# Optimization experiments

Hardware: AMD Instinct MI355X
Metric: run time of the kernel (lower is better)

## Reference

```python
import jax, jax.numpy as jnp
import numpy as np

B, T, E, H = 4, 1024, 1024, 16
D = E // H  # head_dim = 64


def setup_inputs() -> dict:
    key = jax.random.key(0)
    ks = jax.random.split(key, 6)
    s = 0.02  # realistic init scale for stable softmax
    return {
        "hidden_states": jax.random.normal(ks[0], (B, T, E), jnp.float32),
        "attention_mask": jnp.zeros((B, 1, T, T), jnp.float32),
        "Wq": jax.random.normal(ks[1], (E, E), jnp.float32) * s,
        "bq": jnp.zeros((E,), jnp.float32),
        "Wk": jax.random.normal(ks[2], (E, E), jnp.float32) * s,
        "bk": jnp.zeros((E,), jnp.float32),
        "Wv": jax.random.normal(ks[3], (E, E), jnp.float32) * s,
        "bv": jnp.zeros((E,), jnp.float32),
        "Wo": jax.random.normal(ks[4], (E, E), jnp.float32) * s,
        "bo": jnp.zeros((E,), jnp.float32),
    }


def reference(hidden_states, attention_mask, Wq, bq, Wk, bk, Wv, bv, Wo, bo):
    b, t, e = hidden_states.shape
    scaling = jnp.asarray(D, hidden_states.dtype) ** -0.5
    # q_proj weights/bias are pre-scaled in the module; equivalent to scaling q output
    q = (hidden_states @ Wq.T + bq) * scaling      # [B,T,E]
    k = hidden_states @ Wk.T + bk                   # self-attention path (no cache)
    v = hidden_states @ Wv.T + bv
    q = q.reshape(b, t, H, D)
    k = k.reshape(b, t, H, D)
    v = v.reshape(b, t, H, D)
    # bmm(q, k^T): [B,H,T,S] score matrix (materialized, as in the original)
    scores = jnp.einsum("bthd,bshd->bhts", q, k) + attention_mask
    probs = jax.nn.softmax(scores, axis=-1)
    ctx = jnp.einsum("bhts,bshd->bthd", probs, v).reshape(b, t, e)
    return ctx @ Wo.T + bo
```

## Files before the change

kernel.cpp:

```cpp
#include <hip/hip_runtime.h>
#include <math.h>

#define BB 4
#define TT 1024
#define EE 1024
#define HH 16
#define DD 64
#define KDIM 1024
#define N_HS (4096 * 1024)
#define N_W  (1024 * 1024)
#define NQKV (BB * HH * TT * DD)
#define LOG2E 1.44269504088896340736f

typedef _Float16 f16x8 __attribute__((ext_vector_type(8)));
typedef _Float16 f16x4 __attribute__((ext_vector_type(4)));
typedef _Float16 f16x2 __attribute__((ext_vector_type(2)));
typedef float    f32x4 __attribute__((ext_vector_type(4)));

__device__ __forceinline__ unsigned short f2h(float x) {
    _Float16 h = (_Float16)x;
    return __builtin_bit_cast(unsigned short, h);
}
__device__ __forceinline__ void split_h(float x, unsigned short& hi, unsigned short& lo) {
    _Float16 h = (_Float16)x;
    hi = __builtin_bit_cast(unsigned short, h);
    lo = f2h(x - (float)h);
}

__device__ __forceinline__ f16x2 cvt_pk(float a, float b) {
    return __builtin_bit_cast(f16x2, __builtin_amdgcn_cvt_pkrtz(a, b));
}

__device__ __forceinline__ void gload16(const void* g, void* l) {
    __builtin_amdgcn_global_load_lds(
        (const __attribute__((address_space(1))) void*)g,
        (__attribute__((address_space(3))) void*)l, 16, 0, 0);
}

__device__ __forceinline__ float mx3(float a, float b, float c) {
    return fmaxf(fmaxf(a, b), c);
}

__global__ __launch_bounds__(256)
void split_kernel(const float* __restrict__ hs,
                  const float* __restrict__ Wq, const float* __restrict__ Wk,
                  const float* __restrict__ Wv, const float* __restrict__ Wo,
                  const float* __restrict__ mask, int* __restrict__ mflag,
                  unsigned short* __restrict__ ws)
{
    const int u = blockIdx.x * 256 + threadIdx.x;
    if (u < (N_HS / 4) + N_W) {
        const float* src;
        unsigned short* dst;
        if (u < (N_HS / 4)) {
            src = hs + (size_t)u * 4;
            dst = ws + (size_t)u * 4;
        } else {
            int v = u - N_HS / 4;
            int wsel = v >> 18;
            int wo   = v & 0x3FFFF;
            const float* Wsrc = (wsel == 0) ? Wq : (wsel == 1) ? Wk : (wsel == 2) ? Wv : Wo;
            src = Wsrc + (size_t)wo * 4;
            dst = ws + (size_t)N_HS + (size_t)wsel * N_W + (size_t)wo * 4;
        }
        float4 x = *(const float4*)src;
        ushort4 h4;
        h4.x = f2h(x.x); h4.y = f2h(x.y); h4.z = f2h(x.z); h4.w = f2h(x.w);
        *(ushort4*)dst = h4;
    } else {
        int v = u - ((N_HS / 4) + N_W);
        float4 x = *(const float4*)(mask + (size_t)v * 4);
        bool nz = (x.x != 0.f) || (x.y != 0.f) || (x.z != 0.f) || (x.w != 0.f);
        if (__any(nz) && (threadIdx.x & 63) == 0)
            atomicOr(mflag, 1);
    }
}

__global__ __launch_bounds__(256)
void qkv_kernel(const unsigned short* __restrict__ hsp,
                const unsigned short* __restrict__ wqp,
                const float* __restrict__ bq, const float* __restrict__ bk,
                const float* __restrict__ bv,
                unsigned short* __restrict__ qkvb)
{
    __shared__ unsigned short Ah[128 * 32], Bh[128 * 32];

    const int widx  = blockIdx.x >> 3;
    const int nbase = (blockIdx.x & 7) * 128;
    const int mbase = blockIdx.y * 128;
    const unsigned short* Wp = wqp + (size_t)widx * N_W;
    const float* bias = (widx == 0) ? bq : (widx == 1) ? bk : bv;
    unsigned short* dst = qkvb + (size_t)widx * NQKV;
    const float scale = (widx == 0) ? 0.125f * LOG2E : 1.0f;

    const int tid  = threadIdx.x;
    const int w    = tid >> 6;
    const int lane = tid & 63;
    const int quad = lane >> 4;
    const int l16  = lane & 15;
    const int wm   = (w >> 1) * 64;
    const int wn   = (w & 1) * 64;

    f32x4 acc[4][4];
#pragma unroll
    for (int i = 0; i < 4; i++)
#pragma unroll
        for (int j = 0; j < 4; j++) acc[i][j] = (f32x4)0.f;

#pragma unroll 1
    for (int kt = 0; kt < KDIM; kt += 32) {
        __syncthreads();
#pragma unroll
        for (int i = 0; i < 2; i++) {
            int u = tid + i * 256;
            int r = u >> 2, c = u & 3;
            int q = c ^ ((r >> 1) & 3);
            gload16(hsp + (size_t)(mbase + r) * KDIM + kt + q * 8, &Ah[u * 8]);
            gload16(Wp  + (size_t)(nbase + r) * KDIM + kt + q * 8, &Bh[u * 8]);
        }
        __syncthreads();

        f16x8 af[4], bfr[4];
#pragma unroll
        for (int i = 0; i < 4; i++) {
            int r = wm + i * 16 + l16;
            af[i] = *(const f16x8*)&Ah[(r * 4 + (quad ^ ((r >> 1) & 3))) * 8];
        }
#pragma unroll
        for (int j = 0; j < 4; j++) {
            int r = wn + j * 16 + l16;
            bfr[j] = *(const f16x8*)&Bh[(r * 4 + (quad ^ ((r >> 1) & 3))) * 8];
        }
#pragma unroll
        for (int i = 0; i < 4; i++)
#pragma unroll
            for (int j = 0; j < 4; j++)
                acc[i][j] = __builtin_amdgcn_mfma_f32_16x16x32_f16(af[i], bfr[j], acc[i][j], 0, 0, 0);
    }

#pragma unroll
    for (int j = 0; j < 4; j++) {
        int n = nbase + wn + j * 16 + l16;
        int h = n >> 6, d = n & 63;
        float bj = bias[n];
#pragma unroll
        for (int i = 0; i < 4; i++)
#pragma unroll
            for (int rr = 0; rr < 4; rr++) {
                int m = mbase + wm + i * 16 + quad * 4 + rr;
                int b = m >> 10, t = m & 1023;
                dst[(((size_t)(b * HH + h) * TT + t) * DD + d)] =
                    f2h((acc[i][j][rr] + bj) * scale);
            }
    }
}

__global__ __launch_bounds__(256)
void vtrans_kernel(const unsigned short* __restrict__ vp,
                   unsigned short* __restrict__ vtp)
{
    __shared__ unsigned short Ts[64 * 72];
    const int bh = blockIdx.y;
    const int t0 = blockIdx.x * 64;
    const unsigned short* src = vp  + (size_t)bh * TT * DD + (size_t)t0 * DD;
    unsigned short*       dst = vtp + (size_t)bh * DD * TT + t0;
    const int tid = threadIdx.x;

#pragma unroll
    for (int i = 0; i < 2; i++) {
        int id = tid + i * 256;
        int r = id >> 3, c = id & 7;
        *(uint4*)&Ts[r * 72 + c * 8] = *(const uint4*)(src + (size_t)r * DD + c * 8);
    }
    __syncthreads();
#pragma unroll
    for (int i = 0; i < 2; i++) {
        int id = tid + i * 256;
        int d = id >> 3, c = id & 7;
        unsigned short tmp[8];
#pragma unroll
        for (int j = 0; j < 8; j++) tmp[j] = Ts[(c * 8 + j) * 72 + d];
        uint4 o;
        o.x = (unsigned int)tmp[0] | ((unsigned int)tmp[1] << 16);
        o.y = (unsigned int)tmp[2] | ((unsigned int)tmp[3] << 16);
        o.z = (unsigned int)tmp[4] | ((unsigned int)tmp[5] << 16);
        o.w = (unsigned int)tmp[6] | ((unsigned int)tmp[7] << 16);
        *(uint4*)(dst + (size_t)d * TT + c * 8) = o;
    }
}

__global__ __launch_bounds__(256)
void outproj_kernel(const unsigned short* __restrict__ ctxh,
                    const unsigned short* __restrict__ ctxl,
                    const unsigned short* __restrict__ wop,
                    const float* __restrict__ bo, float* __restrict__ out)
{
    __shared__ unsigned short Ach[64 * 32], Acl[64 * 32], Bh[128 * 32];

    const int nbase = blockIdx.x * 128;
    const int mbase = blockIdx.y * 64;

    const int tid  = threadIdx.x;
    const int w    = tid >> 6;
    const int lane = tid & 63;
    const int quad = lane >> 4;
    const int l16  = lane & 15;
    const int wm   = (w >> 1) * 32;
    const int wn   = (w & 1) * 64;

    f32x4 acc[2][4];
#pragma unroll
    for (int i = 0; i < 2; i++)
#pragma unroll
        for (int j = 0; j < 4; j++) acc[i][j] = (f32x4)0.f;

#pragma unroll 1
    for (int kt = 0; kt < KDIM; kt += 32) {
        __syncthreads();
        {
            int r = tid >> 2, c = tid & 3;
            int q = c ^ ((r >> 1) & 3);
            size_t ga = (size_t)(mbase + r) * KDIM + kt + q * 8;
            gload16(ctxh + ga, &Ach[tid * 8]);
            gload16(ctxl + ga, &Acl[tid * 8]);
        }
#pragma unroll
        for (int i = 0; i < 2; i++) {
            int u = tid + i * 256;
            int r = u >> 2, c = u & 3;
            int q = c ^ ((r >> 1) & 3);
            gload16(wop + (size_t)(nbase + r) * KDIM + kt + q * 8, &Bh[u * 8]);
        }
        __syncthreads();

        f16x8 ah[2], al[2], bfr[4];
#pragma unroll
        for (int i = 0; i < 2; i++) {
            int r = wm + i * 16 + l16;
            int slot = (r * 4 + (quad ^ ((r >> 1) & 3))) * 8;
            ah[i] = *(const f16x8*)&Ach[slot];
            al[i] = *(const f16x8*)&Acl[slot];
        }
#pragma unroll
        for (int j = 0; j < 4; j++) {
            int r = wn + j * 16 + l16;
            bfr[j] = *(const f16x8*)&Bh[(r * 4 + (quad ^ ((r >> 1) & 3))) * 8];
        }
#pragma unroll
        for (int i = 0; i < 2; i++)
#pragma unroll
            for (int j = 0; j < 4; j++) {
                acc[i][j] = __builtin_amdgcn_mfma_f32_16x16x32_f16(ah[i], bfr[j], acc[i][j], 0, 0, 0);
                acc[i][j] = __builtin_amdgcn_mfma_f32_16x16x32_f16(al[i], bfr[j], acc[i][j], 0, 0, 0);
            }
    }

#pragma unroll
    for (int j = 0; j < 4; j++) {
        int n = nbase + wn + j * 16 + l16;
        float bj = bo[n];
#pragma unroll
        for (int i = 0; i < 2; i++)
#pragma unroll
            for (int rr = 0; rr < 4; rr++) {
                int m = mbase + wm + i * 16 + quad * 4 + rr;
                out[(size_t)m * EE + n] = acc[i][j][rr] + bj;
            }
    }
}

__global__ __launch_bounds__(256)
void attn_kernel(const unsigned short* __restrict__ qp_, const unsigned short* __restrict__ kp_,
                 const unsigned short* __restrict__ vtp_,
                 const float* __restrict__ mask, const int* __restrict__ mflag,
                 unsigned short* __restrict__ ctxh, unsigned short* __restrict__ ctxl)
{
    __shared__ unsigned short Ks[2][64 * 64];
    __shared__ unsigned short Vt[2][64 * 64];

    const int bh = blockIdx.y;
    const int b  = bh >> 4;
    const int h  = bh & 15;
    const int m0 = blockIdx.x * 64;
    const size_t hoff = (size_t)bh * TT * DD;
    const unsigned short* qhp = qp_ + hoff;
    const unsigned short* khp = kp_ + hoff;
    const unsigned short* vtp = vtp_ + hoff;
    const float* mb = mask + (size_t)b * TT * TT;

    const int tid  = threadIdx.x;
    const int w    = tid >> 6;
    const int lane = tid & 63;
    const int quad = lane >> 4;
    const int l16  = lane & 15;
    const int m    = m0 + w * 16 + l16;

    const int usemask = mflag[0];

    const int lm7 = l16 & 7;
    const int x0  = l16 * 64 + ((quad)     ^ lm7) * 8;
    const int x1  = l16 * 64 + ((4 + quad) ^ lm7) * 8;
    const int qh  = quad >> 1, ql = quad & 1;
    int yy[4];
#pragma unroll
    for (int t = 0; t < 4; t++)
        yy[t] = l16 * 64 + ((2 * t + qh) ^ lm7) * 8 + ql * 4;
    const unsigned short* Ksf = &Ks[0][0];
    const unsigned short* Vtf = &Vt[0][0];

    f16x8 qf[2];
#pragma unroll
    for (int s = 0; s < 2; s++)
        qf[s] = *(const f16x8*)(qhp + (size_t)m * DD + s * 32 + quad * 8);

    f32x4 o2[4];
#pragma unroll
    for (int u = 0; u < 4; u++) o2[u] = (f32x4)0.f;
    f32x4 lv = (f32x4)0.f;
    const f32x4 zc = (f32x4)0.f;
    f16x4 onesv;
    onesv[0] = (_Float16)1.f; onesv[1] = (_Float16)1.f;
    onesv[2] = (_Float16)1.f; onesv[3] = (_Float16)1.f;
    float m_i = -INFINITY;

#pragma unroll
    for (int i = 0; i < 2; i++) {
        int u = tid + i * 256;
        int r = u >> 3, cp = u & 7;
        int c = cp ^ (r & 7);
        gload16(khp + (size_t)r * DD + c * 8, &Ks[0][u * 8]);
        gload16(vtp + (size_t)r * TT + c * 8, &Vt[0][u * 8]);
    }
    __syncthreads();

#pragma unroll 2
    for (int it = 0; it < 16; ++it) {
        const int n0  = it * 64;
        const int cur = it & 1;

        if (it < 15) {
#pragma unroll
            for (int i = 0; i < 2; i++) {
                int u = tid + i * 256;
                int r = u >> 3, cp = u & 7;
                int c = cp ^ (r & 7);
                gload16(khp + (size_t)(n0 + 64 + r) * DD + c * 8, &Ks[cur ^ 1][u * 8]);
                gload16(vtp + (size_t)r * TT + n0 + 64 + c * 8,   &Vt[cur ^ 1][u * 8]);
            }
        }

        f32x4 init[4];
        if (usemask) {
#pragma unroll
            for (int t = 0; t < 4; t++)
#pragma unroll
                for (int r = 0; r < 4; r++)
                    init[t][r] = mb[(size_t)m * TT + n0 + 16 * t + quad * 4 + r] * LOG2E;
        } else {
#pragma unroll
            for (int t = 0; t < 4; t++) init[t] = zc;
        }

        f32x4 st[4];
        __builtin_amdgcn_s_setprio(1);
#pragma unroll
        for (int t = 0; t < 4; t++) {
            const f16x8 kf = *(const f16x8*)(Ksf + cur * 4096 + x0 + t * 1024);
            st[t] = __builtin_amdgcn_mfma_f32_16x16x32_f16(kf, qf[0], init[t], 0, 0, 0);
        }
#pragma unroll
        for (int t = 0; t < 4; t++) {
            const f16x8 kf = *(const f16x8*)(Ksf + cur * 4096 + x1 + t * 1024);
            st[t] = __builtin_amdgcn_mfma_f32_16x16x32_f16(kf, qf[1], st[t], 0, 0, 0);
        }
        __builtin_amdgcn_s_setprio(0);

        float g0 = mx3(st[0][0], st[0][1], st[0][2]);
        float g1 = mx3(st[0][3], st[1][0], st[1][1]);
        float g2 = mx3(st[1][2], st[1][3], st[2][0]);
        float g3 = mx3(st[2][1], st[2][2], st[2][3]);
        float g4 = mx3(st[3][0], st[3][1], st[3][2]);
        float rm = fmaxf(mx3(g0, g1, g2), mx3(g3, g4, st[3][3]));
        rm = fmaxf(rm, __shfl_xor(rm, 16));
        rm = fmaxf(rm, __shfl_xor(rm, 32));

        if (__any(rm > m_i + 8.f)) {
            float mn    = fmaxf(m_i, rm);
            float alpha = exp2f(m_i - mn);
            m_i = mn;
#pragma unroll
            for (int rr = 0; rr < 4; rr++) lv[rr] *= alpha;
#pragma unroll
            for (int u = 0; u < 4; u++)
#pragma unroll
                for (int rr = 0; rr < 4; rr++) o2[u][rr] *= alpha;
        }

        f16x4 pb[4];
#pragma unroll
        for (int t = 0; t < 4; t++) {
            float p0 = exp2f(st[t][0] - m_i);
            float p1 = exp2f(st[t][1] - m_i);
            float p2 = exp2f(st[t][2] - m_i);
            float p3 = exp2f(st[t][3] - m_i);
            f16x2 plo = cvt_pk(p0, p1);
            f16x2 phi = cvt_pk(p2, p3);
            f16x4 pv;
            pv[0] = plo[0]; pv[1] = plo[1]; pv[2] = phi[0]; pv[3] = phi[1];
            pb[t] = pv;
        }

        __builtin_amdgcn_s_setprio(1);
#pragma unroll
        for (int t = 0; t < 4; t++)
            lv = __builtin_amdgcn_mfma_f32_16x16x16f16(onesv, pb[t], lv, 0, 0, 0);
#pragma unroll
        for (int u = 0; u < 4; u++) {
#pragma unroll
            for (int t = 0; t < 4; t++) {
                const f16x4 vv = *(const f16x4*)(Vtf + cur * 4096 + yy[t] + u * 1024);
                o2[u] = __builtin_amdgcn_mfma_f32_16x16x16f16(vv, pb[t], o2[u], 0, 0, 0);
            }
        }
        __builtin_amdgcn_s_setprio(0);

        __syncthreads();
    }

    float inv = 1.0f / lv[0];
#pragma unroll
    for (int u = 0; u < 4; u++)
#pragma unroll
        for (int rr = 0; rr < 4; rr++) {
            float val = o2[u][rr] * inv;
            unsigned short hi, lo;
            split_h(val, hi, lo);
            size_t off = ((size_t)(b * TT + m)) * EE + h * DD + u * 16 + quad * 4 + rr;
            ctxh[off] = hi;
            ctxl[off] = lo;
        }
}

extern "C" void kernel_launch(void* const* d_in, const int* in_sizes, int n_in,
                              void* d_out, int out_size, void* d_ws, size_t ws_size,
                              hipStream_t stream)
{
    const float* hs   = (const float*)d_in[0];
    const float* mask = (const float*)d_in[1];
    const float* Wq   = (const float*)d_in[2];
    const float* bq   = (const float*)d_in[3];
    const float* Wk   = (const float*)d_in[4];
    const float* bk   = (const float*)d_in[5];
    const float* Wv   = (const float*)d_in[6];
    const float* bv   = (const float*)d_in[7];
    const float* Wo   = (const float*)d_in[8];
    const float* bo   = (const float*)d_in[9];
    float* out = (float*)d_out;

    unsigned short* ws   = (unsigned short*)d_ws;
    unsigned short* hsp  = ws;
    unsigned short* wqp  = ws + (size_t)N_HS;
    unsigned short* wop  = wqp + 3 * (size_t)N_W;
    unsigned short* qkvb = wqp + 4 * (size_t)N_W;
    unsigned short* qp   = qkvb;
    unsigned short* kp   = qp + (size_t)NQKV;
    unsigned short* vp   = kp + (size_t)NQKV;
    unsigned short* ctxh = ws;
    unsigned short* ctxl = qkvb + 3 * (size_t)NQKV;
    unsigned short* vtp  = ctxl + (size_t)N_HS;
    int*            mflag = (int*)(vtp + (size_t)NQKV);

    (void)hipMemsetAsync(mflag, 0, sizeof(int), stream);
    split_kernel<<<12288, 256, 0, stream>>>(hs, Wq, Wk, Wv, Wo, mask, mflag, ws);
    qkv_kernel<<<dim3(24, 32), 256, 0, stream>>>(hsp, wqp, bq, bk, bv, qkvb);
    vtrans_kernel<<<dim3(TT / 64, BB * HH), 256, 0, stream>>>(vp, vtp);
    attn_kernel<<<dim3(TT / 64, BB * HH), 256, 0, stream>>>(qp, kp, vtp, mask, mflag, ctxh, ctxl);
    outproj_kernel<<<dim3(8, 64), 256, 0, stream>>>(ctxh, ctxl, wop, bo, out);
}
```

Before: 222.8 us.

## Load K/V fragments directly from global memory and remap blocks per XCD

The attention kernel no longer stages K and V^T tiles in double-buffered shared memory with barriers. Each wave now loads its MFMA operands straight from global memory into registers. The launch becomes a 1D grid whose block index is remapped so that all blocks of one (batch, head) land on the same XCD, which should keep that head's K/V in the shared L2. This removes the LDS traffic and per-iteration __syncthreads. In exchange, all four waves reload the same K/V from cache, register pressure rises, and global load latency is no longer overlapped by explicit prefetch.

```diff
diff --git a/kernel.cpp b/kernel.cpp
--- a/kernel.cpp
+++ b/kernel.cpp
@@ -275,13 +275,12 @@
                  const float* __restrict__ mask, const int* __restrict__ mflag,
                  unsigned short* __restrict__ ctxh, unsigned short* __restrict__ ctxl)
 {
-    __shared__ unsigned short Ks[2][64 * 64];
-    __shared__ unsigned short Vt[2][64 * 64];
-
-    const int bh = blockIdx.y;
+    const int orig = blockIdx.x;
+    const int wgid = (orig & 7) * 128 + (orig >> 3);
+    const int bh = wgid >> 4;
     const int b  = bh >> 4;
     const int h  = bh & 15;
-    const int m0 = blockIdx.x * 64;
+    const int m0 = (wgid & 15) * 64;
     const size_t hoff = (size_t)bh * TT * DD;
     const unsigned short* qhp = qp_ + hoff;
     const unsigned short* khp = kp_ + hoff;
@@ -297,16 +296,8 @@
 
     const int usemask = mflag[0];
 
-    const int lm7 = l16 & 7;
-    const int x0  = l16 * 64 + ((quad)     ^ lm7) * 8;
-    const int x1  = l16 * 64 + ((4 + quad) ^ lm7) * 8;
-    const int qh  = quad >> 1, ql = quad & 1;
-    int yy[4];
-#pragma unroll
-    for (int t = 0; t < 4; t++)
-        yy[t] = l16 * 64 + ((2 * t + qh) ^ lm7) * 8 + ql * 4;
-    const unsigned short* Ksf = &Ks[0][0];
-    const unsigned short* Vtf = &Vt[0][0];
+    const unsigned short* kbase = khp + (size_t)l16 * DD + quad * 8;
+    const unsigned short* vbase = vtp + (size_t)l16 * TT + quad * 4;
 
     f16x8 qf[2];
 #pragma unroll
@@ -323,31 +314,23 @@
     onesv[2] = (_Float16)1.f; onesv[3] = (_Float16)1.f;
     float m_i = -INFINITY;
 
-#pragma unroll
-    for (int i = 0; i < 2; i++) {
-        int u = tid + i * 256;
-        int r = u >> 3, cp = u & 7;
-        int c = cp ^ (r & 7);
-        gload16(khp + (size_t)r * DD + c * 8, &Ks[0][u * 8]);
-        gload16(vtp + (size_t)r * TT + c * 8, &Vt[0][u * 8]);
-    }
-    __syncthreads();
-
 #pragma unroll 2
     for (int it = 0; it < 16; ++it) {
-        const int n0  = it * 64;
-        const int cur = it & 1;
-
-        if (it < 15) {
-#pragma unroll
-            for (int i = 0; i < 2; i++) {
-                int u = tid + i * 256;
-                int r = u >> 3, cp = u & 7;
-                int c = cp ^ (r & 7);
-                gload16(khp + (size_t)(n0 + 64 + r) * DD + c * 8, &Ks[cur ^ 1][u * 8]);
-                gload16(vtp + (size_t)r * TT + n0 + 64 + c * 8,   &Vt[cur ^ 1][u * 8]);
-            }
-        }
+        const int n0 = it * 64;
+
+        f16x8 kf0[4], kf1[4];
+#pragma unroll
+        for (int t = 0; t < 4; t++) {
+            const unsigned short* kr = kbase + (size_t)(n0 + 16 * t) * DD;
+            kf0[t] = *(const f16x8*)(kr);
+            kf1[t] = *(const f16x8*)(kr + 32);
+        }
+        f16x4 vv[4][4];
+#pragma unroll
+        for (int u = 0; u < 4; u++)
+#pragma unroll
+            for (int t = 0; t < 4; t++)
+                vv[u][t] = *(const f16x4*)(vbase + (size_t)(16 * u) * TT + n0 + 16 * t);
 
         f32x4 init[4];
         if (usemask) {
@@ -364,15 +347,11 @@
         f32x4 st[4];
         __builtin_amdgcn_s_setprio(1);
 #pragma unroll
-        for (int t = 0; t < 4; t++) {
-            const f16x8 kf = *(const f16x8*)(Ksf + cur * 4096 + x0 + t * 1024);
-            st[t] = __builtin_amdgcn_mfma_f32_16x16x32_f16(kf, qf[0], init[t], 0, 0, 0);
-        }
-#pragma unroll
-        for (int t = 0; t < 4; t++) {
-            const f16x8 kf = *(const f16x8*)(Ksf + cur * 4096 + x1 + t * 1024);
-            st[t] = __builtin_amdgcn_mfma_f32_16x16x32_f16(kf, qf[1], st[t], 0, 0, 0);
-        }
+        for (int t = 0; t < 4; t++)
+            st[t] = __builtin_amdgcn_mfma_f32_16x16x32_f16(kf0[t], qf[0], init[t], 0, 0, 0);
+#pragma unroll
+        for (int t = 0; t < 4; t++)
+            st[t] = __builtin_amdgcn_mfma_f32_16x16x32_f16(kf1[t], qf[1], st[t], 0, 0, 0);
         __builtin_amdgcn_s_setprio(0);
 
         float g0 = mx3(st[0][0], st[0][1], st[0][2]);
@@ -417,14 +396,10 @@
 #pragma unroll
         for (int u = 0; u < 4; u++) {
 #pragma unroll
-            for (int t = 0; t < 4; t++) {
-                const f16x4 vv = *(const f16x4*)(Vtf + cur * 4096 + yy[t] + u * 1024);
-                o2[u] = __builtin_amdgcn_mfma_f32_16x16x16f16(vv, pb[t], o2[u], 0, 0, 0);
-            }
+            for (int t = 0; t < 4; t++)
+                o2[u] = __builtin_amdgcn_mfma_f32_16x16x16f16(vv[u][t], pb[t], o2[u], 0, 0, 0);
         }
         __builtin_amdgcn_s_setprio(0);
-
-        __syncthreads();
     }
 
     float inv = 1.0f / lv[0];
@@ -474,6 +449,6 @@
     split_kernel<<<12288, 256, 0, stream>>>(hs, Wq, Wk, Wv, Wo, mask, mflag, ws);
     qkv_kernel<<<dim3(24, 32), 256, 0, stream>>>(hsp, wqp, bq, bk, bv, qkvb);
     vtrans_kernel<<<dim3(TT / 64, BB * HH), 256, 0, stream>>>(vp, vtp);
-    attn_kernel<<<dim3(TT / 64, BB * HH), 256, 0, stream>>>(qp, kp, vtp, mask, mflag, ctxh, ctxl);
+    attn_kernel<<<1024, 256, 0, stream>>>(qp, kp, vtp, mask, mflag, ctxh, ctxl);
     outproj_kernel<<<dim3(8, 64), 256, 0, stream>>>(ctxh, ctxl, wop, bo, out);
 }
```

Result: slower. 344.6 us (+54.7%).

## Fuse V transpose into QKV epilogue and deepen attention K/V pipelining

Applied to the files above, without the earlier changes.

The QKV GEMM epilogue now writes V directly in transposed [B,H,D,T] layout using 4-wide stores, removing the separate vtrans kernel launch and its extra pass over V. The attention kernel uses a 4-slot K/V LDS ring that loads two tiles per barrier and processes them in pairs, which halves the number of __syncthreads. It also remaps the 1D grid so that consecutive blocks are spread across heads, likely for XCD/L2 locality. LDS use doubles to 64KB per block, which may lower occupancy.

```diff
diff --git a/kernel.cpp b/kernel.cpp
--- a/kernel.cpp
+++ b/kernel.cpp
@@ -81,7 +81,8 @@
                 const unsigned short* __restrict__ wqp,
                 const float* __restrict__ bq, const float* __restrict__ bk,
                 const float* __restrict__ bv,
-                unsigned short* __restrict__ qkvb)
+                unsigned short* __restrict__ qkvb,
+                unsigned short* __restrict__ vtp)
 {
     __shared__ unsigned short Ah[128 * 32], Bh[128 * 32];
 
@@ -138,54 +139,40 @@
                 acc[i][j] = __builtin_amdgcn_mfma_f32_16x16x32_f16(af[i], bfr[j], acc[i][j], 0, 0, 0);
     }
 
-#pragma unroll
-    for (int j = 0; j < 4; j++) {
-        int n = nbase + wn + j * 16 + l16;
-        int h = n >> 6, d = n & 63;
-        float bj = bias[n];
-#pragma unroll
-        for (int i = 0; i < 4; i++)
-#pragma unroll
-            for (int rr = 0; rr < 4; rr++) {
-                int m = mbase + wm + i * 16 + quad * 4 + rr;
-                int b = m >> 10, t = m & 1023;
-                dst[(((size_t)(b * HH + h) * TT + t) * DD + d)] =
-                    f2h((acc[i][j][rr] + bj) * scale);
-            }
-    }
-}
-
-__global__ __launch_bounds__(256)
-void vtrans_kernel(const unsigned short* __restrict__ vp,
-                   unsigned short* __restrict__ vtp)
-{
-    __shared__ unsigned short Ts[64 * 72];
-    const int bh = blockIdx.y;
-    const int t0 = blockIdx.x * 64;
-    const unsigned short* src = vp  + (size_t)bh * TT * DD + (size_t)t0 * DD;
-    unsigned short*       dst = vtp + (size_t)bh * DD * TT + t0;
-    const int tid = threadIdx.x;
-
-#pragma unroll
-    for (int i = 0; i < 2; i++) {
-        int id = tid + i * 256;
-        int r = id >> 3, c = id & 7;
-        *(uint4*)&Ts[r * 72 + c * 8] = *(const uint4*)(src + (size_t)r * DD + c * 8);
-    }
-    __syncthreads();
-#pragma unroll
-    for (int i = 0; i < 2; i++) {
-        int id = tid + i * 256;
-        int d = id >> 3, c = id & 7;
-        unsigned short tmp[8];
-#pragma unroll
-        for (int j = 0; j < 8; j++) tmp[j] = Ts[(c * 8 + j) * 72 + d];
-        uint4 o;
-        o.x = (unsigned int)tmp[0] | ((unsigned int)tmp[1] << 16);
-        o.y = (unsigned int)tmp[2] | ((unsigned int)tmp[3] << 16);
-        o.z = (unsigned int)tmp[4] | ((unsigned int)tmp[5] << 16);
-        o.w = (unsigned int)tmp[6] | ((unsigned int)tmp[7] << 16);
-        *(uint4*)(dst + (size_t)d * TT + c * 8) = o;
+    if (widx == 2) {
+        const int b  = mbase >> 10;
+        const int tb = (mbase & 1023) + wm + quad * 4;
+#pragma unroll
+        for (int j = 0; j < 4; j++) {
+            int n = nbase + wn + j * 16 + l16;
+            int h = n >> 6, d = n & 63;
+            float bj = bias[n];
+#pragma unroll
+            for (int i = 0; i < 4; i++) {
+                ushort4 vw;
+                vw.x = f2h(acc[i][j][0] + bj);
+                vw.y = f2h(acc[i][j][1] + bj);
+                vw.z = f2h(acc[i][j][2] + bj);
+                vw.w = f2h(acc[i][j][3] + bj);
+                *(ushort4*)(vtp + (((size_t)(b * HH + h) * DD + d) * TT + tb + i * 16)) = vw;
+            }
+        }
+    } else {
+#pragma unroll
+        for (int j = 0; j < 4; j++) {
+            int n = nbase + wn + j * 16 + l16;
+            int h = n >> 6, d = n & 63;
+            float bj = bias[n];
+#pragma unroll
+            for (int i = 0; i < 4; i++)
+#pragma unroll
+                for (int rr = 0; rr < 4; rr++) {
+                    int m = mbase + wm + i * 16 + quad * 4 + rr;
+                    int b = m >> 10, t = m & 1023;
+                    dst[(((size_t)(b * HH + h) * TT + t) * DD + d)] =
+                        f2h((acc[i][j][rr] + bj) * scale);
+                }
+        }
     }
 }
 
@@ -275,13 +262,15 @@
                  const float* __restrict__ mask, const int* __restrict__ mflag,
                  unsigned short* __restrict__ ctxh, unsigned short* __restrict__ ctxl)
 {
-    __shared__ unsigned short Ks[2][64 * 64];
-    __shared__ unsigned short Vt[2][64 * 64];
-
-    const int bh = blockIdx.y;
+    __shared__ unsigned short Ks[4][64 * 64];
+    __shared__ unsigned short Vt[4][64 * 64];
+
+    const int orig = blockIdx.x;
+    const int wgid = (orig & 7) * 128 + (orig >> 3);
+    const int bh = wgid >> 4;
     const int b  = bh >> 4;
     const int h  = bh & 15;
-    const int m0 = blockIdx.x * 64;
+    const int m0 = (wgid & 15) * 64;
     const size_t hoff = (size_t)bh * TT * DD;
     const unsigned short* qhp = qp_ + hoff;
     const unsigned short* khp = kp_ + hoff;
@@ -324,105 +313,117 @@
     float m_i = -INFINITY;
 
 #pragma unroll
-    for (int i = 0; i < 2; i++) {
-        int u = tid + i * 256;
-        int r = u >> 3, cp = u & 7;
-        int c = cp ^ (r & 7);
-        gload16(khp + (size_t)r * DD + c * 8, &Ks[0][u * 8]);
-        gload16(vtp + (size_t)r * TT + c * 8, &Vt[0][u * 8]);
-    }
+    for (int tl = 0; tl < 2; tl++)
+#pragma unroll
+        for (int i = 0; i < 2; i++) {
+            int u = tid + i * 256;
+            int r = u >> 3, cp = u & 7;
+            int c = cp ^ (r & 7);
+            gload16(khp + (size_t)(tl * 64 + r) * DD + c * 8, &Ks[tl][u * 8]);
+            gload16(vtp + (size_t)r * TT + tl * 64 + c * 8,   &Vt[tl][u * 8]);
+        }
     __syncthreads();
 
 #pragma unroll 2
-    for (int it = 0; it < 16; ++it) {
-        const int n0  = it * 64;
-        const int cur = it & 1;
-
-        if (it < 15) {
-#pragma unroll
-            for (int i = 0; i < 2; i++) {
-                int u = tid + i * 256;
-                int r = u >> 3, cp = u & 7;
-                int c = cp ^ (r & 7);
-                gload16(khp + (size_t)(n0 + 64 + r) * DD + c * 8, &Ks[cur ^ 1][u * 8]);
-                gload16(vtp + (size_t)r * TT + n0 + 64 + c * 8,   &Vt[cur ^ 1][u * 8]);
-            }
-        }
-
-        f32x4 init[4];
-        if (usemask) {
+    for (int bi = 0; bi < 8; ++bi) {
+        if (bi < 7) {
+#pragma unroll
+            for (int tl = 0; tl < 2; tl++) {
+                const int tile = 2 * bi + 2 + tl;
+                const int buf  = tile & 3;
+                const int nb   = tile * 64;
+#pragma unroll
+                for (int i = 0; i < 2; i++) {
+                    int u = tid + i * 256;
+                    int r = u >> 3, cp = u & 7;
+                    int c = cp ^ (r & 7);
+                    gload16(khp + (size_t)(nb + r) * DD + c * 8, &Ks[buf][u * 8]);
+                    gload16(vtp + (size_t)r * TT + nb + c * 8,   &Vt[buf][u * 8]);
+                }
+            }
+        }
+
+#pragma unroll
+        for (int half = 0; half < 2; half++) {
+            const int it  = 2 * bi + half;
+            const int buf = it & 3;
+            const int n0  = it * 64;
+
+            f32x4 init[4];
+            if (usemask) {
+#pragma unroll
+                for (int t = 0; t < 4; t++)
+#pragma unroll
+                    for (int r = 0; r < 4; r++)
+                        init[t][r] = mb[(size_t)m * TT + n0 + 16 * t + quad * 4 + r] * LOG2E;
+            } else {
+#pragma unroll
+                for (int t = 0; t < 4; t++) init[t] = zc;
+            }
+
+            f32x4 st[4];
+            __builtin_amdgcn_s_setprio(1);
+#pragma unroll
+            for (int t = 0; t < 4; t++) {
+                const f16x8 kf = *(const f16x8*)(Ksf + buf * 4096 + x0 + t * 1024);
+                st[t] = __builtin_amdgcn_mfma_f32_16x16x32_f16(kf, qf[0], init[t], 0, 0, 0);
+            }
+#pragma unroll
+            for (int t = 0; t < 4; t++) {
+                const f16x8 kf = *(const f16x8*)(Ksf + buf * 4096 + x1 + t * 1024);
+                st[t] = __builtin_amdgcn_mfma_f32_16x16x32_f16(kf, qf[1], st[t], 0, 0, 0);
+            }
+            __builtin_amdgcn_s_setprio(0);
+
+            float g0 = mx3(st[0][0], st[0][1], st[0][2]);
+            float g1 = mx3(st[0][3], st[1][0], st[1][1]);
+            float g2 = mx3(st[1][2], st[1][3], st[2][0]);
+            float g3 = mx3(st[2][1], st[2][2], st[2][3]);
+            float g4 = mx3(st[3][0], st[3][1], st[3][2]);
+            float rm = fmaxf(mx3(g0, g1, g2), mx3(g3, g4, st[3][3]));
+            rm = fmaxf(rm, __shfl_xor(rm, 16));
+            rm = fmaxf(rm, __shfl_xor(rm, 32));
+
+            if (__any(rm > m_i + 8.f)) {
+                float mn    = fmaxf(m_i, rm);
+                float alpha = exp2f(m_i - mn);
+                m_i = mn;
+#pragma unroll
+                for (int rr = 0; rr < 4; rr++) lv[rr] *= alpha;
+#pragma unroll
+                for (int u = 0; u < 4; u++)
+#pragma unroll
+                    for (int rr = 0; rr < 4; rr++) o2[u][rr] *= alpha;
+            }
+
+            f16x4 pb[4];
+#pragma unroll
+            for (int t = 0; t < 4; t++) {
+                float p0 = exp2f(st[t][0] - m_i);
+                float p1 = exp2f(st[t][1] - m_i);
+                float p2 = exp2f(st[t][2] - m_i);
+                float p3 = exp2f(st[t][3] - m_i);
+                f16x2 plo = cvt_pk(p0, p1);
+                f16x2 phi = cvt_pk(p2, p3);
+                f16x4 pv;
+                pv[0] = plo[0]; pv[1] = plo[1]; pv[2] = phi[0]; pv[3] = phi[1];
+                pb[t] = pv;
+            }
+
+            __builtin_amdgcn_s_setprio(1);
 #pragma unroll
             for (int t = 0; t < 4; t++)
-#pragma unroll
-                for (int r = 0; r < 4; r++)
-                    init[t][r] = mb[(size_t)m * TT + n0 + 16 * t + quad * 4 + r] * LOG2E;
-        } else {
-#pragma unroll
-            for (int t = 0; t < 4; t++) init[t] = zc;
-        }
-
-        f32x4 st[4];
-        __builtin_amdgcn_s_setprio(1);
-#pragma unroll
-        for (int t = 0; t < 4; t++) {
-            const f16x8 kf = *(const f16x8*)(Ksf + cur * 4096 + x0 + t * 1024);
-            st[t] = __builtin_amdgcn_mfma_f32_16x16x32_f16(kf, qf[0], init[t], 0, 0, 0);
-        }
-#pragma unroll
-        for (int t = 0; t < 4; t++) {
-            const f16x8 kf = *(const f16x8*)(Ksf + cur * 4096 + x1 + t * 1024);
-            st[t] = __builtin_amdgcn_mfma_f32_16x16x32_f16(kf, qf[1], st[t], 0, 0, 0);
-        }
-        __builtin_amdgcn_s_setprio(0);
-
-        float g0 = mx3(st[0][0], st[0][1], st[0][2]);
-        float g1 = mx3(st[0][3], st[1][0], st[1][1]);
-        float g2 = mx3(st[1][2], st[1][3], st[2][0]);
-        float g3 = mx3(st[2][1], st[2][2], st[2][3]);
-        float g4 = mx3(st[3][0], st[3][1], st[3][2]);
-        float rm = fmaxf(mx3(g0, g1, g2), mx3(g3, g4, st[3][3]));
-        rm = fmaxf(rm, __shfl_xor(rm, 16));
-        rm = fmaxf(rm, __shfl_xor(rm, 32));
-
-        if (__any(rm > m_i + 8.f)) {
-            float mn    = fmaxf(m_i, rm);
-            float alpha = exp2f(m_i - mn);
-            m_i = mn;
-#pragma unroll
-            for (int rr = 0; rr < 4; rr++) lv[rr] *= alpha;
-#pragma unroll
-            for (int u = 0; u < 4; u++)
-#pragma unroll
-                for (int rr = 0; rr < 4; rr++) o2[u][rr] *= alpha;
-        }
-
-        f16x4 pb[4];
-#pragma unroll
-        for (int t = 0; t < 4; t++) {
-            float p0 = exp2f(st[t][0] - m_i);
-            float p1 = exp2f(st[t][1] - m_i);
-            float p2 = exp2f(st[t][2] - m_i);
-            float p3 = exp2f(st[t][3] - m_i);
-            f16x2 plo = cvt_pk(p0, p1);
-            f16x2 phi = cvt_pk(p2, p3);
-            f16x4 pv;
-            pv[0] = plo[0]; pv[1] = plo[1]; pv[2] = phi[0]; pv[3] = phi[1];
-            pb[t] = pv;
-        }
-
-        __builtin_amdgcn_s_setprio(1);
-#pragma unroll
-        for (int t = 0; t < 4; t++)
-            lv = __builtin_amdgcn_mfma_f32_16x16x16f16(onesv, pb[t], lv, 0, 0, 0);
-#pragma unroll
-        for (int u = 0; u < 4; u++) {
-#pragma unroll
-            for (int t = 0; t < 4; t++) {
-                const f16x4 vv = *(const f16x4*)(Vtf + cur * 4096 + yy[t] + u * 1024);
-                o2[u] = __builtin_amdgcn_mfma_f32_16x16x16f16(vv, pb[t], o2[u], 0, 0, 0);
-            }
-        }
-        __builtin_amdgcn_s_setprio(0);
+                lv = __builtin_amdgcn_mfma_f32_16x16x16f16(onesv, pb[t], lv, 0, 0, 0);
+#pragma unroll
+            for (int u = 0; u < 4; u++) {
+#pragma unroll
+                for (int t = 0; t < 4; t++) {
+                    const f16x4 vv = *(const f16x4*)(Vtf + buf * 4096 + yy[t] + u * 1024);
+                    o2[u] = __builtin_amdgcn_mfma_f32_16x16x16f16(vv, pb[t], o2[u], 0, 0, 0);
+                }
+            }
+            __builtin_amdgcn_s_setprio(0);
+        }
 
         __syncthreads();
     }
@@ -464,7 +465,6 @@
     unsigned short* qkvb = wqp + 4 * (size_t)N_W;
     unsigned short* qp   = qkvb;
     unsigned short* kp   = qp + (size_t)NQKV;
-    unsigned short* vp   = kp + (size_t)NQKV;
     unsigned short* ctxh = ws;
     unsigned short* ctxl = qkvb + 3 * (size_t)NQKV;
     unsigned short* vtp  = ctxl + (size_t)N_HS;
@@ -472,8 +472,7 @@
 
     (void)hipMemsetAsync(mflag, 0, sizeof(int), stream);
     split_kernel<<<12288, 256, 0, stream>>>(hs, Wq, Wk, Wv, Wo, mask, mflag, ws);
-    qkv_kernel<<<dim3(24, 32), 256, 0, stream>>>(hsp, wqp, bq, bk, bv, qkvb);
-    vtrans_kernel<<<dim3(TT / 64, BB * HH), 256, 0, stream>>>(vp, vtp);
-    attn_kernel<<<dim3(TT / 64, BB * HH), 256, 0, stream>>>(qp, kp, vtp, mask, mflag, ctxh, ctxl);
+    qkv_kernel<<<dim3(24, 32), 256, 0, stream>>>(hsp, wqp, bq, bk, bv, qkvb, vtp);
+    attn_kernel<<<1024, 256, 0, stream>>>(qp, kp, vtp, mask, mflag, ctxh, ctxl);
     outproj_kernel<<<dim3(8, 64), 256, 0, stream>>>(ctxh, ctxl, wop, bo, out);
 }
```

Result: slower. 233.9 us (+5.0%).
